# Performance work log

Hardware: AMD Instinct MI355X
Metric: run time of the kernel (lower is better)

## Reference

```python
import jax, jax.numpy as jnp
import numpy as np

N_NODES = 100000
N_EDGES = 3200000
D = 256


def setup_inputs() -> dict:
    key = jax.random.key(0)
    k1, k2, k3, k4, k5, k6 = jax.random.split(key, 6)
    embeddings = jax.random.normal(k1, (N_NODES, D), dtype=jnp.float32)
    edge_vals = jax.random.uniform(k2, (N_EDGES,), dtype=jnp.float32)
    # glorot-ish scale for the dense transforms
    scale = 1.0 / np.sqrt(D)
    W1 = jax.random.normal(k3, (D, D), dtype=jnp.float32) * scale
    W2 = jax.random.normal(k4, (D, D), dtype=jnp.float32) * scale
    edge_rows = jax.random.randint(k5, (N_EDGES,), 0, N_NODES, dtype=jnp.int32)
    edge_cols = jax.random.randint(k6, (N_EDGES,), 0, N_NODES, dtype=jnp.int32)
    return {
        "embeddings": embeddings,
        "edge_vals": edge_vals,
        "W1": W1,
        "W2": W2,
        "edge_rows": edge_rows,
        "edge_cols": edge_cols,
    }


def reference(embeddings, edge_vals, W1, W2, edge_rows, edge_cols):
    # SpMM: neighbor_interaction = A @ embeddings, A given as COO (rows, cols, vals)
    gathered = edge_vals[:, None] * embeddings[edge_cols]          # [E, D]
    neighbor = jax.ops.segment_sum(gathered, edge_rows,
                                   num_segments=embeddings.shape[0])  # [N, D]
    # include_self_messages = True branch:
    # self_interaction + neighbor_messages  ==  (emb + neighbor) @ W1
    out = (embeddings + neighbor) @ W1 + (neighbor * embeddings) @ W2
    return out
```

## Files before the change

### kernel.cpp

```cpp
#include <hip/hip_runtime.h>
#include <cstdint>
#include <cstddef>

#define N_NODES 100000
#define N_EDGES 3200000
#define DD 256
#define KK 512
#define MPAD 100096
#define NSCAN 98
#define NGRP 8
#define GRP_ROWS 12500
#define NSLOT 256
#define SLOT_E 12500

typedef __attribute__((ext_vector_type(8))) __bf16 bf16x8;
typedef __attribute__((ext_vector_type(4))) __bf16 bf16x4;
typedef __attribute__((ext_vector_type(4))) float f32x4;

__device__ __forceinline__ void gload_lds16(const void* gsrc, void* lds) {
  __builtin_amdgcn_global_load_lds((const __attribute__((address_space(1))) void*)gsrc,
                                   (__attribute__((address_space(3))) void*)lds,
                                   16, 0, 0);
}


__global__ void conve_kernel(const float* __restrict__ emb, __bf16* __restrict__ embB) {
  int i = blockIdx.x * blockDim.x + threadIdx.x;
  float4 v = ((const float4*)emb)[i];
  bf16x4 o;
  o[0] = (__bf16)v.x; o[1] = (__bf16)v.y; o[2] = (__bf16)v.z; o[3] = (__bf16)v.w;
  ((bf16x4*)embB)[i] = o;
}

__global__ void convw_kernel(const float* __restrict__ W1, const float* __restrict__ W2,
                             __bf16* __restrict__ Wt) {
  int idx = blockIdx.x * blockDim.x + threadIdx.x;
  int n = idx >> 9;
  int k = idx & 511;
  float v = (k < 256) ? W1[k * 256 + n] : W2[(k - 256) * 256 + n];
  Wt[idx] = (__bf16)v;
}


__global__ void zero_ints_kernel(int* __restrict__ p, int n) {
  int i = blockIdx.x * blockDim.x + threadIdx.x;
  if (i < n) p[i] = 0;
}

__global__ void hist_kernel(const int* __restrict__ rows, int* __restrict__ counts) {
  const int g = blockIdx.x & (NGRP - 1);
  const int s = blockIdx.x >> 3;
  const int rlo = g * GRP_ROWS;
  const int rhi = rlo + GRP_ROWS;
  const int base = s * SLOT_E;
  for (int i = base + threadIdx.x; i < base + SLOT_E; i += 256) {
    int r = rows[i];
    if (r >= rlo && r < rhi) atomicAdd(&counts[r], 1);
  }
}

__global__ void scan_block_kernel(const int* __restrict__ counts, int* __restrict__ offsets,
                                  int* __restrict__ blockSums, int n) {
  __shared__ int s[1024];
  int t = threadIdx.x;
  int i = blockIdx.x * 1024 + t;
  int v = (i < n) ? counts[i] : 0;
  s[t] = v;
  __syncthreads();
  for (int off = 1; off < 1024; off <<= 1) {
    int x = (t >= off) ? s[t - off] : 0;
    __syncthreads();
    s[t] += x;
    __syncthreads();
  }
  if (i < n) offsets[i + 1] = s[t];
  if (t == 1023) blockSums[blockIdx.x] = s[1023];
}

__global__ void scan_sums_kernel(const int* __restrict__ blockSums, int* __restrict__ blockBase,
                                 int nb, int* __restrict__ offsets) {
  __shared__ int s[128];
  int t = threadIdx.x;
  int v = (t < nb) ? blockSums[t] : 0;
  s[t] = v;
  __syncthreads();
  for (int off = 1; off < 128; off <<= 1) {
    int x = (t >= off) ? s[t - off] : 0;
    __syncthreads();
    s[t] += x;
    __syncthreads();
  }
  if (t < nb) blockBase[t] = s[t] - v;
  if (t == 0) offsets[0] = 0;
}

__global__ void scan_add_kernel(const int* __restrict__ counts, int* __restrict__ offsets,
                                const int* __restrict__ blockBase, int* __restrict__ cursor, int n) {
  int i = blockIdx.x * 1024 + threadIdx.x;
  if (i < n) {
    int incl = offsets[i + 1] + blockBase[blockIdx.x];
    offsets[i + 1] = incl;
    cursor[i] = incl - counts[i];
  }
}

__global__ void bin_kernel(const int* __restrict__ rows, const int* __restrict__ cols,
                           const float* __restrict__ vals, int* __restrict__ cursor,
                           uint2* __restrict__ sedge) {
  const int g = blockIdx.x & (NGRP - 1);
  const int s = blockIdx.x >> 3;
  const int rlo = g * GRP_ROWS;
  const int rhi = rlo + GRP_ROWS;
  const int base = s * SLOT_E;
  for (int i = base + threadIdx.x; i < base + SLOT_E; i += 256) {
    int r = rows[i];
    if (r >= rlo && r < rhi) {
      int pos = atomicAdd(&cursor[r], 1);
      sedge[pos] = make_uint2((unsigned)cols[i], __float_as_uint(vals[i]));
    }
  }
}


__global__ void spmm_fuse_kernel(const __bf16* __restrict__ embB, const int* __restrict__ offsets,
                                 const uint2* __restrict__ sedge, __bf16* __restrict__ X) {
  int gw = (blockIdx.x << 2) + (threadIdx.x >> 6);
  int lane = threadIdx.x & 63;
  bf16x4* xp1 = (bf16x4*)(X + (size_t)gw * KK + 4 * lane);
  bf16x4* xp2 = (bf16x4*)(X + (size_t)gw * KK + DD + 4 * lane);
  if (gw >= N_NODES) {
    bf16x4 z;
    z[0] = (__bf16)0.f; z[1] = (__bf16)0.f; z[2] = (__bf16)0.f; z[3] = (__bf16)0.f;
    *xp1 = z; *xp2 = z;
    return;
  }
  const bf16x4* ev = (const bf16x4*)embB;
  float ax = 0.f, ay = 0.f, az = 0.f, aw = 0.f;
  int e = offsets[gw];
  const int eend = offsets[gw + 1];
  for (; e + 7 < eend; e += 8) {
    uint2 ee[8];
    bf16x4 xx[8];
#pragma unroll
    for (int u = 0; u < 8; ++u) ee[u] = sedge[e + u];
#pragma unroll
    for (int u = 0; u < 8; ++u) xx[u] = ev[(size_t)ee[u].x * 64 + lane];
#pragma unroll
    for (int u = 0; u < 8; ++u) {
      float v = __uint_as_float(ee[u].y);
      ax = fmaf(v, (float)xx[u][0], ax); ay = fmaf(v, (float)xx[u][1], ay);
      az = fmaf(v, (float)xx[u][2], az); aw = fmaf(v, (float)xx[u][3], aw);
    }
  }
  for (; e + 3 < eend; e += 4) {
    uint2 ee[4];
    bf16x4 xx[4];
#pragma unroll
    for (int u = 0; u < 4; ++u) ee[u] = sedge[e + u];
#pragma unroll
    for (int u = 0; u < 4; ++u) xx[u] = ev[(size_t)ee[u].x * 64 + lane];
#pragma unroll
    for (int u = 0; u < 4; ++u) {
      float v = __uint_as_float(ee[u].y);
      ax = fmaf(v, (float)xx[u][0], ax); ay = fmaf(v, (float)xx[u][1], ay);
      az = fmaf(v, (float)xx[u][2], az); aw = fmaf(v, (float)xx[u][3], aw);
    }
  }
  for (; e < eend; ++e) {
    uint2 ee = sedge[e];
    float v = __uint_as_float(ee.y);
    bf16x4 x = ev[(size_t)ee.x * 64 + lane];
    ax = fmaf(v, (float)x[0], ax); ay = fmaf(v, (float)x[1], ay);
    az = fmaf(v, (float)x[2], az); aw = fmaf(v, (float)x[3], aw);
  }
  bf16x4 er = ev[(size_t)gw * 64 + lane];
  float ex = (float)er[0], ey = (float)er[1], ez = (float)er[2], ew = (float)er[3];
  bf16x4 o1, o2;
  o1[0] = (__bf16)(ex + ax); o1[1] = (__bf16)(ey + ay);
  o1[2] = (__bf16)(ez + az); o1[3] = (__bf16)(ew + aw);
  o2[0] = (__bf16)(ex * ax); o2[1] = (__bf16)(ey * ay);
  o2[2] = (__bf16)(ez * az); o2[3] = (__bf16)(ew * aw);
  *xp1 = o1;
  *xp2 = o2;
}


__global__ __launch_bounds__(256) void gemm_kernel(const __bf16* __restrict__ X,
                                                   const __bf16* __restrict__ Wt,
                                                   float* __restrict__ out) {
  __shared__ __align__(16) __bf16 As[128 * 64];
  __shared__ __align__(16) __bf16 Bs[128 * 64];
  const int t = threadIdx.x;
  const int w = t >> 6, lane = t & 63;
  const int m0 = blockIdx.x * 128;
  const int n0 = blockIdx.y * 128;
  const int wm = (w >> 1) * 64, wn = (w & 1) * 64;
  const int lrow = lane >> 3, lcol = lane & 7;
  const int scol = (lcol ^ lrow) * 8;

  f32x4 acc[4][4];
#pragma unroll
  for (int i = 0; i < 4; ++i)
#pragma unroll
    for (int j = 0; j < 4; ++j) {
      f32x4 z = {0.f, 0.f, 0.f, 0.f};
      acc[i][j] = z;
    }

  for (int kt = 0; kt < KK; kt += 64) {
#pragma unroll
    for (int q = 0; q < 4; ++q) {
      const int cbase = w * 256 + q * 64;
      const int arow = m0 + w * 32 + q * 8 + lrow;
      gload_lds16(X + (size_t)arow * KK + kt + scol, (char*)As + cbase * 16);
      const int brow = n0 + w * 32 + q * 8 + lrow;
      gload_lds16(Wt + (size_t)brow * KK + kt + scol, (char*)Bs + cbase * 16);
    }
    __syncthreads();
    const int l15 = lane & 15, lhi = lane >> 4;
#pragma unroll
    for (int kk = 0; kk < 64; kk += 32) {
      bf16x8 af[4], bg[4];
#pragma unroll
      for (int i = 0; i < 4; ++i) {
        const int ar = wm + i * 16 + l15;
        af[i] = *(const bf16x8*)((const char*)As + ar * 128 +
                                 (((kk + lhi * 8) * 2) ^ ((ar & 7) << 4)));
      }
#pragma unroll
      for (int j = 0; j < 4; ++j) {
        const int br = wn + j * 16 + l15;
        bg[j] = *(const bf16x8*)((const char*)Bs + br * 128 +
                                 (((kk + lhi * 8) * 2) ^ ((br & 7) << 4)));
      }
#pragma unroll
      for (int i = 0; i < 4; ++i)
#pragma unroll
        for (int j = 0; j < 4; ++j)
          acc[i][j] = __builtin_amdgcn_mfma_f32_16x16x32_bf16(af[i], bg[j], acc[i][j], 0, 0, 0);
    }
    __syncthreads();
  }

  const int orow0 = m0 + wm + ((lane >> 4) << 2);
  const int ocol0 = n0 + wn + (lane & 15);
#pragma unroll
  for (int i = 0; i < 4; ++i)
#pragma unroll
    for (int j = 0; j < 4; ++j)
#pragma unroll
      for (int r = 0; r < 4; ++r) {
        const int row = orow0 + i * 16 + r;
        if (row < N_NODES) out[(size_t)row * DD + ocol0 + j * 16] = acc[i][j][r];
      }
}


extern "C" void kernel_launch(void* const* d_in, const int* in_sizes, int n_in,
                              void* d_out, int out_size, void* d_ws, size_t ws_size,
                              hipStream_t stream) {
  const float* emb  = (const float*)d_in[0];
  const float* ev   = (const float*)d_in[1];
  const float* W1   = (const float*)d_in[2];
  const float* W2   = (const float*)d_in[3];
  const int* erows  = (const int*)d_in[4];
  const int* ecols  = (const int*)d_in[5];
  float* out = (float*)d_out;
  char* ws = (char*)d_ws;

  const size_t OFF_X   = 0;
  const size_t OFF_EMB = OFF_X   + (size_t)MPAD * KK * 2;
  const size_t OFF_WT  = OFF_EMB + (size_t)N_NODES * DD * 2;
  const size_t OFF_CNT = OFF_WT  + (size_t)KK * DD * 2;
  const size_t OFF_OFS = OFF_CNT + 401408;
  const size_t OFF_CUR = OFF_OFS + 401408;
  const size_t OFF_BS  = OFF_CUR + 401408;
  const size_t OFF_BB  = OFF_BS  + 4096;
  const size_t OFF_SE  = OFF_BB  + 4096;

  __bf16* X     = (__bf16*)(ws + OFF_X);
  __bf16* embB  = (__bf16*)(ws + OFF_EMB);
  __bf16* Wt    = (__bf16*)(ws + OFF_WT);
  int* counts   = (int*)(ws + OFF_CNT);
  int* offsets  = (int*)(ws + OFF_OFS);
  int* cursor   = (int*)(ws + OFF_CUR);
  int* bsums    = (int*)(ws + OFF_BS);
  int* bbase    = (int*)(ws + OFF_BB);
  uint2* sedge  = (uint2*)(ws + OFF_SE);

  conve_kernel<<<(N_NODES * 64) / 256, 256, 0, stream>>>(emb, embB);
  convw_kernel<<<(KK * DD) / 256, 256, 0, stream>>>(W1, W2, Wt);

  zero_ints_kernel<<<(N_NODES + 255) / 256, 256, 0, stream>>>(counts, N_NODES);
  hist_kernel<<<NGRP * NSLOT, 256, 0, stream>>>(erows, counts);
  scan_block_kernel<<<NSCAN, 1024, 0, stream>>>(counts, offsets, bsums, N_NODES);
  scan_sums_kernel<<<1, 128, 0, stream>>>(bsums, bbase, NSCAN, offsets);
  scan_add_kernel<<<NSCAN, 1024, 0, stream>>>(counts, offsets, bbase, cursor, N_NODES);
  bin_kernel<<<NGRP * NSLOT, 256, 0, stream>>>(erows, ecols, ev, cursor, sedge);

  spmm_fuse_kernel<<<MPAD / 4, 256, 0, stream>>>(embB, offsets, sedge, X);

  gemm_kernel<<<dim3(MPAD / 128, 2), 256, 0, stream>>>(X, Wt, out);

  (void)in_sizes; (void)n_in; (void)out_size; (void)ws_size;
}
```

Baseline: 766.7 us.

## Pre-bucketize edges by row group before histogram and binning

Adds a bucketize pass that splits edges into 64 segments, one per row group and block class, with coalesced writes through shared memory. The histogram and bin kernels then read only their own group's edges instead of each scanning all edges 8 times and filtering by row range. This cuts redundant global reads and improves atomic locality per group. The cost is an extra pass writing 3 arrays into the X workspace region. It also relies on a fixed per-segment capacity, which random row indices are expected not to exceed.

```diff
diff --git a/kernel.cpp b/kernel.cpp
--- a/kernel.cpp
+++ b/kernel.cpp
@@ -10,8 +10,7 @@
 #define NSCAN 98
 #define NGRP 8
 #define GRP_ROWS 12500
-#define NSLOT 256
-#define SLOT_E 12500
+#define SEGCAP 53248
 
 typedef __attribute__((ext_vector_type(8))) __bf16 bf16x8;
 typedef __attribute__((ext_vector_type(4))) __bf16 bf16x4;
@@ -47,16 +46,60 @@
   if (i < n) p[i] = 0;
 }
 
-__global__ void hist_kernel(const int* __restrict__ rows, int* __restrict__ counts) {
-  const int g = blockIdx.x & (NGRP - 1);
+__global__ __launch_bounds__(256) void bucketize_kernel(
+    const int* __restrict__ rows, const int* __restrict__ cols, const float* __restrict__ vals,
+    int* __restrict__ gcur, uint32_t* __restrict__ br, uint32_t* __restrict__ bc,
+    float* __restrict__ bv) {
+  __shared__ int s_cnt[8];
+  __shared__ int s_base[8];
+  __shared__ uint32_t s_r[8][256];
+  __shared__ uint32_t s_c[8][256];
+  __shared__ float s_v[8][256];
+  const int tid = threadIdx.x;
+  const int x = blockIdx.x & 7;
+  if (tid < 8) s_cnt[tid] = 0;
+  __syncthreads();
+  for (int e0 = blockIdx.x * 256; e0 < N_EDGES; e0 += gridDim.x * 256) {
+    const int i = e0 + tid;
+    if (i < N_EDGES) {
+      const int r = rows[i];
+      const int g = r / GRP_ROWS;
+      const int idx = atomicAdd(&s_cnt[g], 1);
+      s_r[g][idx] = (uint32_t)r;
+      s_c[g][idx] = (uint32_t)cols[i];
+      s_v[g][idx] = vals[i];
+    }
+    __syncthreads();
+    if (tid < 8) s_base[tid] = atomicAdd(&gcur[x * 16 + tid], s_cnt[tid]);
+    __syncthreads();
+#pragma unroll
+    for (int g = 0; g < 8; ++g) {
+      const int cnt = s_cnt[g];
+      const size_t dst0 = (size_t)(g * 8 + x) * SEGCAP + s_base[g];
+      for (int k = tid; k < cnt; k += 256) {
+        br[dst0 + k] = s_r[g][k];
+        bc[dst0 + k] = s_c[g][k];
+        bv[dst0 + k] = s_v[g][k];
+      }
+    }
+    __syncthreads();
+    if (tid < 8) s_cnt[tid] = 0;
+    __syncthreads();
+  }
+}
+
+__global__ void histg_kernel(const uint32_t* __restrict__ br, const int* __restrict__ gcur,
+                             int* __restrict__ counts) {
+  const int g = blockIdx.x & 7;
   const int s = blockIdx.x >> 3;
-  const int rlo = g * GRP_ROWS;
-  const int rhi = rlo + GRP_ROWS;
-  const int base = s * SLOT_E;
-  for (int i = base + threadIdx.x; i < base + SLOT_E; i += 256) {
-    int r = rows[i];
-    if (r >= rlo && r < rhi) atomicAdd(&counts[r], 1);
-  }
+  const int x = s & 7;
+  const int c = s >> 3;
+  const int len = gcur[x * 16 + g];
+  const int cl = (len + 31) >> 5;
+  const int lo = c * cl;
+  const int hi = (lo + cl < len) ? lo + cl : len;
+  const uint32_t* p = br + (size_t)(g * 8 + x) * SEGCAP;
+  for (int i = lo + threadIdx.x; i < hi; i += 256) atomicAdd(&counts[p[i]], 1);
 }
 
 __global__ void scan_block_kernel(const int* __restrict__ counts, int* __restrict__ offsets,
@@ -104,20 +147,22 @@
   }
 }
 
-__global__ void bin_kernel(const int* __restrict__ rows, const int* __restrict__ cols,
-                           const float* __restrict__ vals, int* __restrict__ cursor,
-                           uint2* __restrict__ sedge) {
-  const int g = blockIdx.x & (NGRP - 1);
+__global__ void bin2_kernel(const uint32_t* __restrict__ br, const uint32_t* __restrict__ bc,
+                            const float* __restrict__ bv, const int* __restrict__ gcur,
+                            int* __restrict__ cursor, uint2* __restrict__ sedge) {
+  const int g = blockIdx.x & 7;
   const int s = blockIdx.x >> 3;
-  const int rlo = g * GRP_ROWS;
-  const int rhi = rlo + GRP_ROWS;
-  const int base = s * SLOT_E;
-  for (int i = base + threadIdx.x; i < base + SLOT_E; i += 256) {
-    int r = rows[i];
-    if (r >= rlo && r < rhi) {
-      int pos = atomicAdd(&cursor[r], 1);
-      sedge[pos] = make_uint2((unsigned)cols[i], __float_as_uint(vals[i]));
-    }
+  const int x = s & 7;
+  const int c = s >> 3;
+  const int len = gcur[x * 16 + g];
+  const int cl = (len + 31) >> 5;
+  const int lo = c * cl;
+  const int hi = (lo + cl < len) ? lo + cl : len;
+  const size_t seg = (size_t)(g * 8 + x) * SEGCAP;
+  for (int i = lo + threadIdx.x; i < hi; i += 256) {
+    const int r = (int)br[seg + i];
+    const int pos = atomicAdd(&cursor[r], 1);
+    sedge[pos] = make_uint2(bc[seg + i], __float_as_uint(bv[seg + i]));
   }
 }
 
@@ -269,9 +314,13 @@
   char* ws = (char*)d_ws;
 
   const size_t OFF_X   = 0;
+  const size_t OFF_BR  = OFF_X;
+  const size_t OFF_BC  = OFF_BR + (size_t)64 * SEGCAP * 4;
+  const size_t OFF_BV  = OFF_BC + (size_t)64 * SEGCAP * 4;
   const size_t OFF_EMB = OFF_X   + (size_t)MPAD * KK * 2;
   const size_t OFF_WT  = OFF_EMB + (size_t)N_NODES * DD * 2;
   const size_t OFF_CNT = OFF_WT  + (size_t)KK * DD * 2;
+  const size_t OFF_GC  = OFF_CNT + 400000;
   const size_t OFF_OFS = OFF_CNT + 401408;
   const size_t OFF_CUR = OFF_OFS + 401408;
   const size_t OFF_BS  = OFF_CUR + 401408;
@@ -279,9 +328,13 @@
   const size_t OFF_SE  = OFF_BB  + 4096;
 
   __bf16* X     = (__bf16*)(ws + OFF_X);
+  uint32_t* br  = (uint32_t*)(ws + OFF_BR);
+  uint32_t* bc  = (uint32_t*)(ws + OFF_BC);
+  float* bv     = (float*)(ws + OFF_BV);
   __bf16* embB  = (__bf16*)(ws + OFF_EMB);
   __bf16* Wt    = (__bf16*)(ws + OFF_WT);
   int* counts   = (int*)(ws + OFF_CNT);
+  int* gcur     = (int*)(ws + OFF_GC);
   int* offsets  = (int*)(ws + OFF_OFS);
   int* cursor   = (int*)(ws + OFF_CUR);
   int* bsums    = (int*)(ws + OFF_BS);
@@ -291,12 +344,13 @@
   conve_kernel<<<(N_NODES * 64) / 256, 256, 0, stream>>>(emb, embB);
   convw_kernel<<<(KK * DD) / 256, 256, 0, stream>>>(W1, W2, Wt);
 
-  zero_ints_kernel<<<(N_NODES + 255) / 256, 256, 0, stream>>>(counts, N_NODES);
-  hist_kernel<<<NGRP * NSLOT, 256, 0, stream>>>(erows, counts);
+  zero_ints_kernel<<<(100128 + 255) / 256, 256, 0, stream>>>(counts, 100128);
+  bucketize_kernel<<<2048, 256, 0, stream>>>(erows, ecols, ev, gcur, br, bc, bv);
+  histg_kernel<<<2048, 256, 0, stream>>>(br, gcur, counts);
   scan_block_kernel<<<NSCAN, 1024, 0, stream>>>(counts, offsets, bsums, N_NODES);
   scan_sums_kernel<<<1, 128, 0, stream>>>(bsums, bbase, NSCAN, offsets);
   scan_add_kernel<<<NSCAN, 1024, 0, stream>>>(counts, offsets, bbase, cursor, N_NODES);
-  bin_kernel<<<NGRP * NSLOT, 256, 0, stream>>>(erows, ecols, ev, cursor, sedge);
+  bin2_kernel<<<2048, 256, 0, stream>>>(br, bc, bv, gcur, cursor, sedge);
 
   spmm_fuse_kernel<<<MPAD / 4, 256, 0, stream>>>(embB, offsets, sedge, X);
 
```

New measurement: 784.9 us. 1.02x slower.
